# Optimization experiments

Measured on AMD Instinct MI355X. Metric: run time of the kernel, lower is better.

## Reference

```python
import jax, jax.numpy as jnp
import numpy as np

N_NODES = 256
N_SECRETS = 64
N_INPUTS = 16      # per-node source-node inputs
N_SECDEP = 8       # per-node secret-dependency columns
ENTRIES = 3 + N_INPUTS + N_SECDEP  # 27
ACTION_SIZE = 4096
BATCH = 8192
STATE_DIM = N_NODES + N_SECRETS + 2  # 322


def _build_index_matrix() -> np.ndarray:
    """idx[i] = column indices of `state` concatenated for node i, mirroring split()."""
    rng = np.random.default_rng(1234)
    idx = np.empty((N_NODES, ENTRIES), dtype=np.int32)
    g0 = N_NODES + N_SECRETS  # first of the two global columns
    for i in range(N_NODES):
        src = rng.integers(0, N_NODES, size=N_INPUTS)           # inputs[j].sourceNodeIndex
        sec = N_NODES + rng.choice(N_SECRETS, size=N_SECDEP, replace=False)  # secrIndex[i]
        idx[i] = np.concatenate(([i, g0, g0 + 1], src, np.sort(sec)))
    return idx


def setup_inputs() -> dict:
    key = jax.random.key(0)
    k1, k2, k3, k4 = jax.random.split(key, 4)
    state = jax.random.normal(k1, (BATCH, STATE_DIM), dtype=jnp.float32)
    # per-node Linear(ENTRIES, 1): weight [N, E], bias [N]
    bound = 1.0 / np.sqrt(ENTRIES)
    W = jax.random.uniform(k2, (N_NODES, ENTRIES), jnp.float32, -bound, bound)
    b = jax.random.uniform(k3, (N_NODES,), jnp.float32, -bound, bound)
    # final Linear(N_NODES, ACTION_SIZE, bias=False): weight [A, N]
    bf = 1.0 / np.sqrt(N_NODES)
    Wf = jax.random.uniform(k4, (ACTION_SIZE, N_NODES), jnp.float32, -bf, bf)
    idx = jnp.asarray(_build_index_matrix())
    return {"state": state, "W": W, "b": b, "Wf": Wf, "idx": idx}


def reference(state, W, b, Wf, idx):
    # split(): per-node gather of ENTRIES columns -> [B, N, E]
    gathered = jnp.take(state, idx, axis=1)
    # per-node tiny Linear + tanh -> [B, N]
    y = jnp.tanh(jnp.einsum("bne,ne->bn", gathered, W) + b)
    # final linear (no bias), scaled sigmoid -> [B, A]
    return 500.0 * jax.nn.sigmoid(jnp.einsum("bn,an->ba", y, Wf))
```

## Files before the change

kernel.cpp:

```cpp
#include <hip/hip_runtime.h>
#include <hip/hip_bf16.h>

#define N_NODES 256
#define ENTRIES 27
#define ACTION 4096
#define BATCH 8192
#define SDIM 322

typedef unsigned short u16;
typedef u16 u16x4 __attribute__((ext_vector_type(4)));
typedef u16 u16x8 __attribute__((ext_vector_type(8)));
typedef __bf16 bf16x8 __attribute__((ext_vector_type(8)));
typedef float floatx4 __attribute__((ext_vector_type(4)));

__device__ __forceinline__ u16 f2bf(float f) {
    unsigned u = __builtin_bit_cast(unsigned, f);
    unsigned r = (u + 0x7FFFu + ((u >> 16) & 1u)) >> 16;
    return (u16)r;
}

__global__ __launch_bounds__(256) void node_kernel(
    const float* __restrict__ state, const float* __restrict__ W,
    const float* __restrict__ bias, const int* __restrict__ idx,
    u16* __restrict__ y)
{
    __shared__ float srow[8 * SDIM];
    const int n  = threadIdx.x;
    const int b0 = blockIdx.x * 8;

    for (int i = threadIdx.x; i < 8 * SDIM; i += 256) {
        int r = i / SDIM;
        int c = i - r * SDIM;
        srow[i] = state[(size_t)(b0 + r) * SDIM + c];
    }

    int   ix[ENTRIES];
    float w [ENTRIES];
#pragma unroll
    for (int e = 0; e < ENTRIES; e++) {
        ix[e] = idx[n * ENTRIES + e];
        w [e] = W  [n * ENTRIES + e];
    }
    const float bb = bias[n];
    __syncthreads();

#pragma unroll
    for (int r = 0; r < 8; r++) {
        const float* sp = &srow[r * SDIM];
        float s = bb;
#pragma unroll
        for (int e = 0; e < ENTRIES; e++) s += sp[ix[e]] * w[e];
        y[(size_t)(b0 + r) * N_NODES + n] = f2bf(tanhf(s));
    }
}

__global__ __launch_bounds__(256) void conv_kernel(
    const float* __restrict__ wf, u16* __restrict__ out)
{
    const int i0 = (blockIdx.x * 256 + threadIdx.x) * 4;
    floatx4 v = *(const floatx4*)(wf + i0);
    u16x4 r;
    r.x = f2bf(v.x); r.y = f2bf(v.y); r.z = f2bf(v.z); r.w = f2bf(v.w);
    *(u16x4*)(out + i0) = r;
}

__global__ __launch_bounds__(256) void gemm_kernel(
    const u16* __restrict__ Y, const u16* __restrict__ WF,
    float* __restrict__ out)
{
    __shared__ u16 As[128 * 32];
    __shared__ u16 Bs[128 * 32];

    const int bm   = blockIdx.x;
    const int bn   = blockIdx.y;
    const int tid  = threadIdx.x;
    const int lane = tid & 63;
    const int wave = tid >> 6;
    const int wm   = wave & 1;
    const int wn   = wave >> 1;

    const int l15  = lane & 15;
    const int koff = (lane >> 4) << 3;

    floatx4 acc[4][4];
#pragma unroll
    for (int mi = 0; mi < 4; mi++)
#pragma unroll
        for (int ni = 0; ni < 4; ni++)
            acc[mi][ni] = (floatx4){0.f, 0.f, 0.f, 0.f};

    const size_t arow0 = (size_t)bm * 128;
    const size_t brow0 = (size_t)bn * 128;

    for (int kk = 0; kk < 256; kk += 32) {
        __syncthreads();
#pragma unroll
        for (int c = tid; c < 512; c += 256) {
            int row = c >> 2;
            int k8  = (c & 3) << 3;
            *(u16x8*)&As[c * 8] =
                *(const u16x8*)&Y [(arow0 + row) * 256 + kk + k8];
            *(u16x8*)&Bs[c * 8] =
                *(const u16x8*)&WF[(brow0 + row) * 256 + kk + k8];
        }
        __syncthreads();

        bf16x8 afrag[4], bfrag[4];
#pragma unroll
        for (int mi = 0; mi < 4; mi++)
            afrag[mi] = __builtin_bit_cast(bf16x8,
                *(const u16x8*)&As[((wm << 6) + (mi << 4) + l15) * 32 + koff]);
#pragma unroll
        for (int ni = 0; ni < 4; ni++)
            bfrag[ni] = __builtin_bit_cast(bf16x8,
                *(const u16x8*)&Bs[((wn << 6) + (ni << 4) + l15) * 32 + koff]);

#pragma unroll
        for (int mi = 0; mi < 4; mi++)
#pragma unroll
            for (int ni = 0; ni < 4; ni++)
                acc[mi][ni] = __builtin_amdgcn_mfma_f32_16x16x32_bf16(
                    afrag[mi], bfrag[ni], acc[mi][ni], 0, 0, 0);
    }

    const int r0 = (lane >> 4) << 2;
#pragma unroll
    for (int mi = 0; mi < 4; mi++) {
#pragma unroll
        for (int ni = 0; ni < 4; ni++) {
            const int row = bm * 128 + wm * 64 + mi * 16 + r0;
            const int col = bn * 128 + wn * 64 + ni * 16 + l15;
#pragma unroll
            for (int r = 0; r < 4; r++) {
                float v = acc[mi][ni][r];
                out[(size_t)(row + r) * ACTION + col] =
                    500.0f / (1.0f + __expf(-v));
            }
        }
    }
}

extern "C" void kernel_launch(void* const* d_in, const int* in_sizes, int n_in,
                              void* d_out, int out_size, void* d_ws, size_t ws_size,
                              hipStream_t stream) {
    const float* state = (const float*)d_in[0];
    const float* W     = (const float*)d_in[1];
    const float* b     = (const float*)d_in[2];
    const float* Wf    = (const float*)d_in[3];
    const int*   idx   = (const int*)  d_in[4];
    float* out = (float*)d_out;

    u16* y   = (u16*)d_ws;
    u16* wfb = y + (size_t)BATCH * N_NODES;

    node_kernel<<<BATCH / 8, 256, 0, stream>>>(state, W, b, idx, y);
    conv_kernel<<<(ACTION * N_NODES / 4) / 256, 256, 0, stream>>>(Wf, wfb);
    gemm_kernel<<<dim3(BATCH / 128, ACTION / 128), 256, 0, stream>>>(y, wfb, out);
}
```

Measured before the change: 186.2 us.

## Recast per-node gather-linear as dense bf16 GEMM and use direct global-to-LDS loads

The gather plus per-node tiny linear is rewritten as a dense matmul: the per-node weights are scattered into a zero-padded [256 x 352] matrix, state is converted to padded bf16, and an MFMA GEMM with a bias+tanh epilogue produces y. The GEMM tile loads now use global_load_lds to copy straight into shared memory without passing through registers. This swaps the LDS-gather node kernel for tensor-core work but adds two conversion kernels and rounds state to bf16, which loses precision on the first stage.

```diff
diff --git a/kernel.cpp b/kernel.cpp
--- a/kernel.cpp
+++ b/kernel.cpp
@@ -1,11 +1,13 @@
 #include <hip/hip_runtime.h>
 #include <hip/hip_bf16.h>
+#include <cmath>
 
-#define N_NODES 256
 #define ENTRIES 27
-#define ACTION 4096
-#define BATCH 8192
-#define SDIM 322
+#define ACTION  4096
+#define BATCH   8192
+#define SDIM    322
+#define KPAD    352
+#define NNODES  256
 
 typedef unsigned short u16;
 typedef u16 u16x4 __attribute__((ext_vector_type(4)));
@@ -19,42 +21,41 @@
     return (u16)r;
 }
 
-__global__ __launch_bounds__(256) void node_kernel(
-    const float* __restrict__ state, const float* __restrict__ W,
-    const float* __restrict__ bias, const int* __restrict__ idx,
-    u16* __restrict__ y)
-{
-    __shared__ float srow[8 * SDIM];
-    const int n  = threadIdx.x;
-    const int b0 = blockIdx.x * 8;
-
-    for (int i = threadIdx.x; i < 8 * SDIM; i += 256) {
-        int r = i / SDIM;
-        int c = i - r * SDIM;
-        srow[i] = state[(size_t)(b0 + r) * SDIM + c];
-    }
-
-    int   ix[ENTRIES];
-    float w [ENTRIES];
-#pragma unroll
-    for (int e = 0; e < ENTRIES; e++) {
-        ix[e] = idx[n * ENTRIES + e];
-        w [e] = W  [n * ENTRIES + e];
-    }
-    const float bb = bias[n];
-    __syncthreads();
-
-#pragma unroll
-    for (int r = 0; r < 8; r++) {
-        const float* sp = &srow[r * SDIM];
-        float s = bb;
-#pragma unroll
-        for (int e = 0; e < ENTRIES; e++) s += sp[ix[e]] * w[e];
-        y[(size_t)(b0 + r) * N_NODES + n] = f2bf(tanhf(s));
-    }
+__device__ __forceinline__ void gl_lds16(const u16* g, u16* l) {
+    __builtin_amdgcn_global_load_lds(
+        (const __attribute__((address_space(1))) unsigned int*)g,
+        (__attribute__((address_space(3))) unsigned int*)l, 16, 0, 0);
 }
 
-__global__ __launch_bounds__(256) void conv_kernel(
+__global__ __launch_bounds__(256) void build_wg(
+    const float* __restrict__ W, const int* __restrict__ idx,
+    u16* __restrict__ wg)
+{
+    __shared__ float rows[32 * KPAD];
+    const int tid = threadIdx.x;
+    for (int i = tid; i < 32 * KPAD; i += 256) rows[i] = 0.f;
+    __syncthreads();
+    if (tid < 32) {
+        const int n = blockIdx.x * 32 + tid;
+        for (int e = 0; e < ENTRIES; e++)
+            rows[tid * KPAD + idx[n * ENTRIES + e]] += W[n * ENTRIES + e];
+    }
+    __syncthreads();
+    for (int i = tid; i < 32 * KPAD; i += 256)
+        wg[(size_t)blockIdx.x * 32 * KPAD + i] = f2bf(rows[i]);
+}
+
+__global__ __launch_bounds__(256) void conv_state(
+    const float* __restrict__ s, u16* __restrict__ o)
+{
+    const int i = blockIdx.x * 256 + threadIdx.x;
+    const int b = i / KPAD;
+    const int c = i - b * KPAD;
+    float v = (c < SDIM) ? s[(size_t)b * SDIM + c] : 0.f;
+    o[i] = f2bf(v);
+}
+
+__global__ __launch_bounds__(256) void conv_wf(
     const float* __restrict__ wf, u16* __restrict__ out)
 {
     const int i0 = (blockIdx.x * 256 + threadIdx.x) * 4;
@@ -64,9 +65,10 @@
     *(u16x4*)(out + i0) = r;
 }
 
-__global__ __launch_bounds__(256) void gemm_kernel(
-    const u16* __restrict__ Y, const u16* __restrict__ WF,
-    float* __restrict__ out)
+template<int KDIM, int EPI>
+__global__ __launch_bounds__(256) void gemm_mfma(
+    const u16* __restrict__ A, const u16* __restrict__ B,
+    void* __restrict__ outp, const float* __restrict__ bias)
 {
     __shared__ u16 As[128 * 32];
     __shared__ u16 Bs[128 * 32];
@@ -78,7 +80,6 @@
     const int wave = tid >> 6;
     const int wm   = wave & 1;
     const int wn   = wave >> 1;
-
     const int l15  = lane & 15;
     const int koff = (lane >> 4) << 3;
 
@@ -89,30 +90,29 @@
         for (int ni = 0; ni < 4; ni++)
             acc[mi][ni] = (floatx4){0.f, 0.f, 0.f, 0.f};
 
-    const size_t arow0 = (size_t)bm * 128;
-    const size_t brow0 = (size_t)bn * 128;
+    const int srow = wave * 32 + (lane >> 2);
+    const int ksub = (lane & 3) << 3;
+    const u16* ga = A + ((size_t)bm * 128 + srow) * KDIM + ksub;
+    const u16* gb = B + ((size_t)bn * 128 + srow) * KDIM + ksub;
+    u16* la = &As[(wave * 32) * 32];
+    u16* lb = &Bs[(wave * 32) * 32];
 
-    for (int kk = 0; kk < 256; kk += 32) {
+    for (int kk = 0; kk < KDIM; kk += 32) {
         __syncthreads();
-#pragma unroll
-        for (int c = tid; c < 512; c += 256) {
-            int row = c >> 2;
-            int k8  = (c & 3) << 3;
-            *(u16x8*)&As[c * 8] =
-                *(const u16x8*)&Y [(arow0 + row) * 256 + kk + k8];
-            *(u16x8*)&Bs[c * 8] =
-                *(const u16x8*)&WF[(brow0 + row) * 256 + kk + k8];
-        }
+        gl_lds16(ga + kk,                  la);
+        gl_lds16(ga + kk + 16 * KDIM,      la + 16 * 32);
+        gl_lds16(gb + kk,                  lb);
+        gl_lds16(gb + kk + 16 * KDIM,      lb + 16 * 32);
         __syncthreads();
 
-        bf16x8 afrag[4], bfrag[4];
+        bf16x8 af[4], bf[4];
 #pragma unroll
         for (int mi = 0; mi < 4; mi++)
-            afrag[mi] = __builtin_bit_cast(bf16x8,
+            af[mi] = __builtin_bit_cast(bf16x8,
                 *(const u16x8*)&As[((wm << 6) + (mi << 4) + l15) * 32 + koff]);
 #pragma unroll
         for (int ni = 0; ni < 4; ni++)
-            bfrag[ni] = __builtin_bit_cast(bf16x8,
+            bf[ni] = __builtin_bit_cast(bf16x8,
                 *(const u16x8*)&Bs[((wn << 6) + (ni << 4) + l15) * 32 + koff]);
 
 #pragma unroll
@@ -120,10 +120,16 @@
 #pragma unroll
             for (int ni = 0; ni < 4; ni++)
                 acc[mi][ni] = __builtin_amdgcn_mfma_f32_16x16x32_bf16(
-                    afrag[mi], bfrag[ni], acc[mi][ni], 0, 0, 0);
+                    af[mi], bf[ni], acc[mi][ni], 0, 0, 0);
     }
 
     const int r0 = (lane >> 4) << 2;
+    float bv[4];
+    if (EPI == 1) {
+#pragma unroll
+        for (int ni = 0; ni < 4; ni++)
+            bv[ni] = bias[bn * 128 + wn * 64 + ni * 16 + l15];
+    }
 #pragma unroll
     for (int mi = 0; mi < 4; mi++) {
 #pragma unroll
@@ -133,8 +139,13 @@
 #pragma unroll
             for (int r = 0; r < 4; r++) {
                 float v = acc[mi][ni][r];
-                out[(size_t)(row + r) * ACTION + col] =
-                    500.0f / (1.0f + __expf(-v));
+                if (EPI == 0) {
+                    ((float*)outp)[(size_t)(row + r) * ACTION + col] =
+                        500.0f / (1.0f + __expf(-v));
+                } else {
+                    ((u16*)outp)[(size_t)(row + r) * NNODES + col] =
+                        f2bf(tanhf(v + bv[ni]));
+                }
             }
         }
     }
@@ -150,10 +161,16 @@
     const int*   idx   = (const int*)  d_in[4];
     float* out = (float*)d_out;
 
-    u16* y   = (u16*)d_ws;
-    u16* wfb = y + (size_t)BATCH * N_NODES;
+    u16* sbf = (u16*)d_ws;
+    u16* wg  = sbf + (size_t)BATCH * KPAD;
+    u16* y   = wg  + (size_t)NNODES * KPAD;
+    u16* wfb = y   + (size_t)BATCH * NNODES;
 
-    node_kernel<<<BATCH / 8, 256, 0, stream>>>(state, W, b, idx, y);
-    conv_kernel<<<(ACTION * N_NODES / 4) / 256, 256, 0, stream>>>(Wf, wfb);
-    gemm_kernel<<<dim3(BATCH / 128, ACTION / 128), 256, 0, stream>>>(y, wfb, out);
+    build_wg  <<<NNODES / 32, 256, 0, stream>>>(W, idx, wg);
+    conv_state<<<BATCH * KPAD / 256, 256, 0, stream>>>(state, sbf);
+    conv_wf   <<<ACTION * NNODES / 1024, 256, 0, stream>>>(Wf, wfb);
+    gemm_mfma<KPAD, 1><<<dim3(BATCH / 128, NNODES / 128), 256, 0, stream>>>(
+        sbf, wg, (void*)y, b);
+    gemm_mfma<256, 0><<<dim3(BATCH / 128, ACTION / 128), 256, 0, stream>>>(
+        y, wfb, (void*)out, nullptr);
 }
```

Result: slower. 190.5 us (+2.3%).
